# Kernel optimization log

Measured on AMD Instinct MI355X. Metric: run time of the kernel, lower is better.

## Reference

```python
import jax, jax.numpy as jnp
import numpy as np

N = 100000
F = 128
H = 4
C = 32
E = 1600000
LEAKY_ALPHA = 0.2


def setup_inputs() -> dict:
    key = jax.random.key(0)
    k1, k2, k3, k4, k5 = jax.random.split(key, 5)
    x = jax.random.normal(k1, (N, F), dtype=jnp.float32)
    edge_index = jax.random.randint(k2, (E, 2), 0, N, dtype=jnp.int64)  # cols: (source, target)
    kernel = jax.random.normal(k3, (F, H, C), dtype=jnp.float32) * 0.05
    attn_kernel_self = jax.random.normal(k4, (C, H), dtype=jnp.float32) * 0.05
    attn_kernel_neighs = jax.random.normal(k5, (C, H), dtype=jnp.float32) * 0.05
    bias = jnp.zeros((H * C,), dtype=jnp.float32)
    return {"x": x, "edge_index": edge_index, "kernel": kernel,
            "attn_kernel_self": attn_kernel_self,
            "attn_kernel_neighs": attn_kernel_neighs, "bias": bias}


def _gat_forward(x, edge_index, kernel, attn_kernel_self, attn_kernel_neighs, bias):
    n = x.shape[0]
    # add self loops: append (i, i) for every node
    loops = jnp.arange(n, dtype=edge_index.dtype)
    indices = jnp.concatenate([edge_index, jnp.stack([loops, loops], axis=1)], axis=0)
    sources, targets = indices[:, 0], indices[:, 1]

    xp = jnp.einsum('nf,fhc->nhc', x, kernel)                 # [N,H,C]
    attn_self = jnp.einsum('nhc,ch->nh', xp, attn_kernel_self)    # [N,H]
    attn_neigh = jnp.einsum('nhc,ch->nh', xp, attn_kernel_neighs)  # [N,H]

    logits = attn_self[targets] + attn_neigh[sources]          # [Etot,H]
    logits = jnp.where(logits >= 0, logits, LEAKY_ALPHA * logits)  # leaky_relu(0.2)

    # segment softmax over targets (every node has a self loop -> no empty segments)
    seg_max = jax.ops.segment_max(logits, targets, num_segments=n)
    e = jnp.exp(logits - seg_max[targets])
    seg_sum = jax.ops.segment_sum(e, targets, num_segments=n)
    alpha = e / seg_sum[targets]                               # [Etot,H]

    # weighted aggregation (dropout is identity at inference)
    msgs = alpha[..., None] * xp[sources]                      # [Etot,H,C]
    out = jax.ops.segment_sum(msgs, targets, num_segments=n)   # [N,H,C]

    out = out.reshape(n, H * C) + bias                         # concat heads + bias, linear activation
    return out, alpha[..., None]


def reference(x, edge_index, kernel, attn_kernel_self, attn_kernel_neighs, bias):
    return _gat_forward(x, edge_index, kernel, attn_kernel_self, attn_kernel_neighs, bias)
```

## Files before the change

kernel.cpp:

```cpp
#include <hip/hip_runtime.h>
#include <hip/hip_bf16.h>
#include <math.h>

#define LEAKY(x) ((x) >= 0.0f ? (x) : 0.2f * (x))
#define CHUNK 8192

typedef __attribute__((ext_vector_type(8))) short short8;
typedef __attribute__((ext_vector_type(4))) float f32x4;

__device__ __forceinline__ float bf_lo(uint32_t u) { return __uint_as_float(u << 16); }
__device__ __forceinline__ float bf_hi(uint32_t u) { return __uint_as_float(u & 0xffff0000u); }
__device__ __forceinline__ uint32_t pack2(float a, float b) {
    __hip_bfloat162 h = __float22bfloat162_rn(make_float2(a, b));
    return *reinterpret_cast<uint32_t*>(&h);
}

__global__ __launch_bounds__(256) void w_prep(
    const float* __restrict__ W, uint32_t* __restrict__ Wp)
{
    const int slot = blockIdx.x * 256 + threadIdx.x;
    if (slot >= 2048) return;
    const int kb = slot >> 9;
    const int cb = (slot >> 6) & 7;
    const int l  = slot & 63;
    const int k0 = kb * 32 + (l >> 4) * 8;
    const int col = cb * 16 + (l & 15);
    uint32_t u[4];
    #pragma unroll
    for (int p = 0; p < 4; ++p) {
        const float a = W[(size_t)(k0 + 2 * p) * 128 + col];
        const float b = W[(size_t)(k0 + 2 * p + 1) * 128 + col];
        u[p] = pack2(a, b);
    }
    *(uint4*)&Wp[(size_t)slot * 4] = make_uint4(u[0], u[1], u[2], u[3]);
}

__global__ __launch_bounds__(256) void gemm_xp(
    const float* __restrict__ x, const uint32_t* __restrict__ Wp,
    const float* __restrict__ aks, const float* __restrict__ akn,
    uint32_t* __restrict__ xpb, float* __restrict__ attn_self,
    float* __restrict__ attn_nei, int N)
{
    __shared__ float xs[64][133];
    const int t  = threadIdx.x;
    const int w  = t >> 6;
    const int l  = t & 63;
    const int nb = blockIdx.x * 64;

    const int row  = nb + w * 16 + (l & 15);
    const int rowc = min(row, N - 1);
    const int kg   = (l >> 4) * 8;
    const float* xrow = x + (size_t)rowc * 128 + kg;

    f32x4 acc[8] = {};
    #pragma unroll
    for (int kb = 0; kb < 4; ++kb) {
        const float4 x0 = *(const float4*)(xrow + kb * 32);
        const float4 x1 = *(const float4*)(xrow + kb * 32 + 4);
        union { short8 s; uint32_t u[4]; } A;
        A.u[0] = pack2(x0.x, x0.y); A.u[1] = pack2(x0.z, x0.w);
        A.u[2] = pack2(x1.x, x1.y); A.u[3] = pack2(x1.z, x1.w);
        #pragma unroll
        for (int cb = 0; cb < 8; ++cb) {
            union { short8 s; uint4 u; } B;
            B.u = *(const uint4*)&Wp[(((size_t)(kb * 8 + cb)) * 64 + l) * 4];
            acc[cb] = __builtin_amdgcn_mfma_f32_16x16x32_bf16(A.s, B.s, acc[cb], 0, 0, 0);
        }
    }

    const int r0 = (l >> 4) * 4;
    const int cl = l & 15;
    #pragma unroll
    for (int cb = 0; cb < 8; ++cb)
        #pragma unroll
        for (int r = 0; r < 4; ++r)
            xs[w * 16 + r0 + r][cb * 16 + cl] = acc[cb][r];
    __syncthreads();

    #pragma unroll
    for (int i = 0; i < 16; ++i) {
        const int idx = t + i * 256;
        const int n = idx >> 6, q = idx & 63;
        const int gn = nb + n;
        if (gn < N)
            xpb[(size_t)gn * 64 + q] = pack2(xs[n][2 * q], xs[n][2 * q + 1]);
    }

    {
        const int n = t & 63, h = t >> 6;
        const int gn = nb + n;
        if (gn < N) {
            float ss = 0.0f, sn = 0.0f;
            #pragma unroll
            for (int c = 0; c < 32; ++c) {
                const float v = xs[n][h * 32 + c];
                ss = fmaf(v, aks[c * 4 + h], ss);
                sn = fmaf(v, akn[c * 4 + h], sn);
            }
            attn_self[(size_t)gn * 4 + h] = ss;
            attn_nei [(size_t)gn * 4 + h] = sn;
        }
    }
}

__global__ __launch_bounds__(256) void binA(
    const int* __restrict__ ei, int2* __restrict__ stage,
    int* __restrict__ start_table, int* __restrict__ bucket_tot,
    int NB, int E)
{
    __shared__ int lh[512], lex[512], ss[256];
    const int t    = threadIdx.x;
    const int base = blockIdx.x * CHUNK;
    const int end  = min(E, base + CHUNK);

    for (int i = t; i < 512; i += 256) lh[i] = 0;
    __syncthreads();
    for (int i = base + t; i < end; i += 256)
        atomicAdd(&lh[((const int2*)ei)[i].y >> 8], 1);
    __syncthreads();

    const int v0 = lh[2 * t], v1 = lh[2 * t + 1];
    ss[t] = v0 + v1;
    __syncthreads();
    for (int d = 1; d < 256; d <<= 1) {
        const int add = (t >= d) ? ss[t - d] : 0;
        __syncthreads();
        ss[t] += add;
        __syncthreads();
    }
    const int ex = ss[t] - v0 - v1;
    lex[2 * t] = ex;
    lex[2 * t + 1] = ex + v0;
    __syncthreads();

    const size_t cbase = (size_t)blockIdx.x * (NB + 1);
    for (int b = t; b <= NB; b += 256) start_table[cbase + b] = base + lex[b];
    for (int b = t; b < NB; b += 256)
        if (lh[b]) atomicAdd(&bucket_tot[b], lh[b]);
    __syncthreads();

    for (int i = base + t; i < end; i += 256) {
        const int2 e2 = ((const int2*)ei)[i];
        const int slot = atomicAdd(&lex[e2.y >> 8], 1);
        stage[base + slot] = e2;
    }
}

__global__ __launch_bounds__(256) void bucket_scan(
    const int* __restrict__ bucket_tot, int* __restrict__ bucket_off,
    int* __restrict__ offsets, int NB, int N, int E)
{
    __shared__ int ss[256];
    const int t = threadIdx.x;
    const int v0 = (2 * t     < NB) ? bucket_tot[2 * t]     : 0;
    const int v1 = (2 * t + 1 < NB) ? bucket_tot[2 * t + 1] : 0;
    ss[t] = v0 + v1;
    __syncthreads();
    for (int d = 1; d < 256; d <<= 1) {
        const int add = (t >= d) ? ss[t - d] : 0;
        __syncthreads();
        ss[t] += add;
        __syncthreads();
    }
    const int ex = ss[t] - v0 - v1;
    if (2 * t     <= NB) bucket_off[2 * t]     = ex;
    if (2 * t + 1 <= NB) bucket_off[2 * t + 1] = ex + v0;
    if (t == 0) offsets[N] = E;
}

__global__ __launch_bounds__(256) void binB(
    const int2* __restrict__ stage, const int* __restrict__ start_table,
    const int* __restrict__ bucket_off, int* __restrict__ offsets,
    int* __restrict__ csr_src, int nc, int NB, int N)
{
    __shared__ int s0[256], cum[257], ss[256], lcnt[256], lcur[256];
    const int t  = threadIdx.x;
    const int b  = blockIdx.x;
    const int lo = b << 8;
    const int nn = min(N, lo + 256) - lo;

    int len = 0;
    if (t < nc) {
        const size_t cb = (size_t)t * (NB + 1);
        const int a0 = start_table[cb + b];
        s0[t] = a0;
        len   = start_table[cb + b + 1] - a0;
    }
    ss[t] = len;
    lcnt[t] = 0;
    __syncthreads();
    for (int d = 1; d < 256; d <<= 1) {
        const int add = (t >= d) ? ss[t - d] : 0;
        __syncthreads();
        ss[t] += add;
        __syncthreads();
    }
    if (t == 0) cum[0] = 0;
    cum[t + 1] = ss[t];
    __syncthreads();
    const int T = cum[nc];

    for (int g = t; g < T; g += 256) {
        int loc = 0, hic = nc - 1;
        while (loc < hic) {
            const int mid = (loc + hic + 1) >> 1;
            if (cum[mid] <= g) loc = mid; else hic = mid - 1;
        }
        const int2 e = stage[s0[loc] + (g - cum[loc])];
        atomicAdd(&lcnt[e.y - lo], 1);
    }
    __syncthreads();

    const int v = lcnt[t];
    ss[t] = v;
    __syncthreads();
    for (int d = 1; d < 256; d <<= 1) {
        const int add = (t >= d) ? ss[t - d] : 0;
        __syncthreads();
        ss[t] += add;
        __syncthreads();
    }
    const int nodeoff = bucket_off[b] + ss[t] - v;
    lcur[t] = nodeoff;
    if (t < nn) offsets[lo + t] = nodeoff;
    __syncthreads();

    for (int g = t; g < T; g += 256) {
        int loc = 0, hic = nc - 1;
        while (loc < hic) {
            const int mid = (loc + hic + 1) >> 1;
            if (cum[mid] <= g) loc = mid; else hic = mid - 1;
        }
        const int2 e = stage[s0[loc] + (g - cum[loc])];
        const int slot = atomicAdd(&lcur[e.y - lo], 1);
        csr_src[slot] = e.x;
    }
}

__global__ __launch_bounds__(256) void aggregate(
    const int* __restrict__ csr_src, const int* __restrict__ offsets,
    const uint32_t* __restrict__ xpb, const float* __restrict__ attn_self,
    const float* __restrict__ attn_nei, const float* __restrict__ bias,
    float* __restrict__ out, float* __restrict__ alpha_out,
    float* __restrict__ inv_arr, int N, int E)
{
    const int lane = threadIdx.x & 63;
    int node = blockIdx.x * 4 + (threadIdx.x >> 6);
    if (node >= N) return;
    node = __builtin_amdgcn_readfirstlane(node);

    const int hL = lane >> 4;
    const int c0 = 2 * lane;

    const float asH = attn_self[(size_t)node * 4 + hL];
    const float anH = attn_nei [(size_t)node * 4 + hL];
    const float eS  = __expf(LEAKY(asH + anH));
    float sumE = eS;
    const uint32_t uS = xpb[(size_t)node * 64 + lane];
    float acc0 = eS * bf_lo(uS), acc1 = eS * bf_hi(uS);

    const int off0 = __builtin_amdgcn_readfirstlane(offsets[node]);
    const int deg  = __builtin_amdgcn_readfirstlane(offsets[node + 1]) - off0;
    const int* srcp = csr_src + off0;

    for (int j = 0; j < deg; j += 4) {
        const int i1 = min(j + 1, deg - 1);
        const int i2 = min(j + 2, deg - 1);
        const int i3 = min(j + 3, deg - 1);
        const int s0 = srcp[j], s1 = srcp[i1], s2 = srcp[i2], s3 = srcp[i3];
        const float a0 = attn_nei[(size_t)s0 * 4 + hL];
        const float a1 = attn_nei[(size_t)s1 * 4 + hL];
        const float a2 = attn_nei[(size_t)s2 * 4 + hL];
        const float a3 = attn_nei[(size_t)s3 * 4 + hL];
        const uint32_t u0 = xpb[(size_t)s0 * 64 + lane];
        const uint32_t u1 = xpb[(size_t)s1 * 64 + lane];
        const uint32_t u2 = xpb[(size_t)s2 * 64 + lane];
        const uint32_t u3 = xpb[(size_t)s3 * 64 + lane];
        const float v0 = __expf(LEAKY(asH + a0));
        const float v1 = (j + 1 < deg) ? __expf(LEAKY(asH + a1)) : 0.0f;
        const float v2 = (j + 2 < deg) ? __expf(LEAKY(asH + a2)) : 0.0f;
        const float v3 = (j + 3 < deg) ? __expf(LEAKY(asH + a3)) : 0.0f;
        sumE += (v0 + v1) + (v2 + v3);
        acc0 = fmaf(v0, bf_lo(u0), acc0); acc1 = fmaf(v0, bf_hi(u0), acc1);
        acc0 = fmaf(v1, bf_lo(u1), acc0); acc1 = fmaf(v1, bf_hi(u1), acc1);
        acc0 = fmaf(v2, bf_lo(u2), acc0); acc1 = fmaf(v2, bf_hi(u2), acc1);
        acc0 = fmaf(v3, bf_lo(u3), acc0); acc1 = fmaf(v3, bf_hi(u3), acc1);
    }

    const float inv = 1.0f / sumE;
    *(float2*)&out[(size_t)node * 128 + c0] =
        make_float2(fmaf(acc0, inv, bias[c0]), fmaf(acc1, inv, bias[c0 + 1]));
    if ((lane & 15) == 0) {
        inv_arr[(size_t)node * 4 + hL] = inv;
        alpha_out[(size_t)(E + node) * 4 + hL] = eS * inv;
    }
}

__global__ __launch_bounds__(256) void alpha_kernel(
    const int* __restrict__ ei, const float* __restrict__ attn_self,
    const float* __restrict__ attn_nei, const float* __restrict__ inv_arr,
    float* __restrict__ alpha_out, int E)
{
    const int i = blockIdx.x * 256 + threadIdx.x;
    if (i >= E) return;
    const int2 e2 = ((const int2*)ei)[i];
    const int src = e2.x, tgt = e2.y;
    const float4 as4 = *(const float4*)&attn_self[(size_t)tgt * 4];
    const float4 an4 = *(const float4*)&attn_nei[(size_t)src * 4];
    const float4 iv4 = *(const float4*)&inv_arr[(size_t)tgt * 4];
    float4 a;
    a.x = __expf(LEAKY(as4.x + an4.x)) * iv4.x;
    a.y = __expf(LEAKY(as4.y + an4.y)) * iv4.y;
    a.z = __expf(LEAKY(as4.z + an4.z)) * iv4.z;
    a.w = __expf(LEAKY(as4.w + an4.w)) * iv4.w;
    *(float4*)&alpha_out[(size_t)i * 4] = a;
}

extern "C" void kernel_launch(void* const* d_in, const int* in_sizes, int n_in,
                              void* d_out, int out_size, void* d_ws, size_t ws_size,
                              hipStream_t stream)
{
    const float* x    = (const float*)d_in[0];
    const int*   ei   = (const int*)d_in[1];
    const float* W    = (const float*)d_in[2];
    const float* aks  = (const float*)d_in[3];
    const float* akn  = (const float*)d_in[4];
    const float* bias = (const float*)d_in[5];

    const int N  = in_sizes[0] / 128;
    const int E  = in_sizes[1] / 2;
    const int NB = (N + 255) >> 8;
    const int nc = (E + CHUNK - 1) / CHUNK;

    float* out       = (float*)d_out;
    float* alpha_out = out + (size_t)N * 128;
    int2* stage      = (int2*)alpha_out;

    char* p = (char*)d_ws;
    auto alloc = [&](size_t bytes) {
        char* r = p;
        p += (bytes + 255) & ~(size_t)255;
        return r;
    };
    uint32_t* xpb       = (uint32_t*)alloc((size_t)N * 64 * 4);
    uint32_t* Wp        = (uint32_t*)alloc((size_t)2048 * 16);
    float* attn_self    = (float*)alloc((size_t)N * 4 * 4);
    float* attn_nei     = (float*)alloc((size_t)N * 4 * 4);
    float* inv_arr      = (float*)alloc((size_t)N * 4 * 4);
    int*   offsets      = (int*)alloc((size_t)(N + 1) * 4);
    int*   csr_src      = (int*)alloc((size_t)E * 4);
    int*   bucket_tot   = (int*)alloc((size_t)NB * 4);
    int*   bucket_off   = (int*)alloc((size_t)(NB + 1) * 4);
    int*   start_table  = (int*)alloc((size_t)nc * (NB + 1) * 4);

    hipMemsetAsync(bucket_tot, 0, (size_t)NB * 4, stream);

    w_prep<<<8, 256, 0, stream>>>(W, Wp);
    gemm_xp<<<(N + 63) / 64, 256, 0, stream>>>(x, Wp, aks, akn, xpb,
                                               attn_self, attn_nei, N);
    binA<<<nc, 256, 0, stream>>>(ei, stage, start_table, bucket_tot, NB, E);
    bucket_scan<<<1, 256, 0, stream>>>(bucket_tot, bucket_off, offsets, NB, N, E);
    binB<<<NB, 256, 0, stream>>>(stage, start_table, bucket_off, offsets,
                                 csr_src, nc, NB, N);
    aggregate<<<(N + 3) / 4, 256, 0, stream>>>(csr_src, offsets, xpb,
                                               attn_self, attn_nei, bias, out,
                                               alpha_out, inv_arr, N, E);
    alpha_kernel<<<(E + 255) / 256, 256, 0, stream>>>(ei, attn_self, attn_nei,
                                                      inv_arr, alpha_out, E);
}
```

Measured before the change: 207.3 us.

## Split wave into four edge groups with 16-byte row loads and shuffle reduction

The aggregate kernel now has each wave split into four 16-lane groups. Each group processes a different neighbor edge and loads the full 256-byte bf16 row with uint4 loads, 8 channels per lane. Partial accumulators and exp sums are combined across groups with xor shuffles at the end. This aims to raise memory-level parallelism and use wider gathers per edge, at the cost of extra shuffle reductions and more wasted lanes on low-degree tail iterations.

```diff
diff --git a/kernel.cpp b/kernel.cpp
--- a/kernel.cpp
+++ b/kernel.cpp
@@ -249,50 +249,67 @@
     if (node >= N) return;
     node = __builtin_amdgcn_readfirstlane(node);
 
-    const int hL = lane >> 4;
-    const int c0 = 2 * lane;
+    const int g  = lane >> 4;
+    const int li = lane & 15;
+    const int hL = li >> 2;
+    const int q0 = li * 4;
 
     const float asH = attn_self[(size_t)node * 4 + hL];
     const float anH = attn_nei [(size_t)node * 4 + hL];
     const float eS  = __expf(LEAKY(asH + anH));
-    float sumE = eS;
-    const uint32_t uS = xpb[(size_t)node * 64 + lane];
-    float acc0 = eS * bf_lo(uS), acc1 = eS * bf_hi(uS);
+
+    const float es0 = (g == 0) ? eS : 0.0f;
+    const uint4 uS = *(const uint4*)&xpb[(size_t)node * 64 + q0];
+    float acc[8];
+    acc[0] = es0 * bf_lo(uS.x); acc[1] = es0 * bf_hi(uS.x);
+    acc[2] = es0 * bf_lo(uS.y); acc[3] = es0 * bf_hi(uS.y);
+    acc[4] = es0 * bf_lo(uS.z); acc[5] = es0 * bf_hi(uS.z);
+    acc[6] = es0 * bf_lo(uS.w); acc[7] = es0 * bf_hi(uS.w);
+    float sumE = es0;
 
     const int off0 = __builtin_amdgcn_readfirstlane(offsets[node]);
     const int deg  = __builtin_amdgcn_readfirstlane(offsets[node + 1]) - off0;
     const int* srcp = csr_src + off0;
 
     for (int j = 0; j < deg; j += 4) {
-        const int i1 = min(j + 1, deg - 1);
-        const int i2 = min(j + 2, deg - 1);
-        const int i3 = min(j + 3, deg - 1);
-        const int s0 = srcp[j], s1 = srcp[i1], s2 = srcp[i2], s3 = srcp[i3];
-        const float a0 = attn_nei[(size_t)s0 * 4 + hL];
-        const float a1 = attn_nei[(size_t)s1 * 4 + hL];
-        const float a2 = attn_nei[(size_t)s2 * 4 + hL];
-        const float a3 = attn_nei[(size_t)s3 * 4 + hL];
-        const uint32_t u0 = xpb[(size_t)s0 * 64 + lane];
-        const uint32_t u1 = xpb[(size_t)s1 * 64 + lane];
-        const uint32_t u2 = xpb[(size_t)s2 * 64 + lane];
-        const uint32_t u3 = xpb[(size_t)s3 * 64 + lane];
-        const float v0 = __expf(LEAKY(asH + a0));
-        const float v1 = (j + 1 < deg) ? __expf(LEAKY(asH + a1)) : 0.0f;
-        const float v2 = (j + 2 < deg) ? __expf(LEAKY(asH + a2)) : 0.0f;
-        const float v3 = (j + 3 < deg) ? __expf(LEAKY(asH + a3)) : 0.0f;
-        sumE += (v0 + v1) + (v2 + v3);
-        acc0 = fmaf(v0, bf_lo(u0), acc0); acc1 = fmaf(v0, bf_hi(u0), acc1);
-        acc0 = fmaf(v1, bf_lo(u1), acc0); acc1 = fmaf(v1, bf_hi(u1), acc1);
-        acc0 = fmaf(v2, bf_lo(u2), acc0); acc1 = fmaf(v2, bf_hi(u2), acc1);
-        acc0 = fmaf(v3, bf_lo(u3), acc0); acc1 = fmaf(v3, bf_hi(u3), acc1);
+        const int e   = j + g;
+        const int idx = min(e, deg - 1);
+        const int s   = srcp[idx];
+        const float an = attn_nei[(size_t)s * 4 + hL];
+        const uint4 u  = *(const uint4*)&xpb[(size_t)s * 64 + q0];
+        const float v  = (e < deg) ? __expf(LEAKY(asH + an)) : 0.0f;
+        sumE += v;
+        acc[0] = fmaf(v, bf_lo(u.x), acc[0]); acc[1] = fmaf(v, bf_hi(u.x), acc[1]);
+        acc[2] = fmaf(v, bf_lo(u.y), acc[2]); acc[3] = fmaf(v, bf_hi(u.y), acc[3]);
+        acc[4] = fmaf(v, bf_lo(u.z), acc[4]); acc[5] = fmaf(v, bf_hi(u.z), acc[5]);
+        acc[6] = fmaf(v, bf_lo(u.w), acc[6]); acc[7] = fmaf(v, bf_hi(u.w), acc[7]);
+    }
+
+    #pragma unroll
+    for (int d = 16; d < 64; d <<= 1) {
+        sumE += __shfl_xor(sumE, d);
+        #pragma unroll
+        for (int k = 0; k < 8; ++k) acc[k] += __shfl_xor(acc[k], d);
     }
 
     const float inv = 1.0f / sumE;
-    *(float2*)&out[(size_t)node * 128 + c0] =
-        make_float2(fmaf(acc0, inv, bias[c0]), fmaf(acc1, inv, bias[c0 + 1]));
-    if ((lane & 15) == 0) {
-        inv_arr[(size_t)node * 4 + hL] = inv;
-        alpha_out[(size_t)(E + node) * 4 + hL] = eS * inv;
+    if (g == 0) {
+        const int c0 = li * 8;
+        float4 o0, o1;
+        o0.x = fmaf(acc[0], inv, bias[c0 + 0]);
+        o0.y = fmaf(acc[1], inv, bias[c0 + 1]);
+        o0.z = fmaf(acc[2], inv, bias[c0 + 2]);
+        o0.w = fmaf(acc[3], inv, bias[c0 + 3]);
+        o1.x = fmaf(acc[4], inv, bias[c0 + 4]);
+        o1.y = fmaf(acc[5], inv, bias[c0 + 5]);
+        o1.z = fmaf(acc[6], inv, bias[c0 + 6]);
+        o1.w = fmaf(acc[7], inv, bias[c0 + 7]);
+        *(float4*)&out[(size_t)node * 128 + c0]     = o0;
+        *(float4*)&out[(size_t)node * 128 + c0 + 4] = o1;
+        if ((li & 3) == 0) {
+            inv_arr[(size_t)node * 4 + hL] = inv;
+            alpha_out[(size_t)(E + node) * 4 + hL] = eS * inv;
+        }
     }
 }
 
```

New measurement: 211.0 us. About the same (+1.8%).
